# Kernel optimization log

Measured on AMD Instinct MI355X. Metric: run time of the kernel, lower is better.

The kernel has to match this reference:

```python
import jax, jax.numpy as jnp
import numpy as np

N = 100000   # nodes
E = 1600000  # edges (avg degree 16)
D = 128      # in_dim == hidden_dim (required by residual + shared BN)
G = 64       # graphs in the batch
EPS = 1e-5   # BatchNorm eps


def setup_inputs() -> dict:
    key = jax.random.key(0)
    ks = jax.random.split(key, 10)
    h = jax.random.normal(ks[0], (N, D), jnp.float32)
    src = jax.random.randint(ks[1], (E,), 0, N)
    dst = jax.random.randint(ks[2], (E,), 0, N)
    graph_ids = jnp.sort(jax.random.randint(ks[3], (N,), 0, G))
    s = 1.0 / np.sqrt(D)
    W1 = jax.random.uniform(ks[4], (D, D), jnp.float32, -s, s)
    b1 = jnp.zeros((D,), jnp.float32)
    W2 = jax.random.uniform(ks[5], (D, D), jnp.float32, -s, s)
    b2 = jnp.zeros((D,), jnp.float32)
    gate_W = jax.random.uniform(ks[6], (D, 1), jnp.float32, -s, s)
    gate_b = jnp.zeros((1,), jnp.float32)
    gamma = jnp.ones((D,), jnp.float32)
    beta = jnp.zeros((D,), jnp.float32)
    return {"h": h, "src": src, "dst": dst, "graph_ids": graph_ids,
            "num_graphs": G, "W1": W1, "b1": b1, "W2": W2, "b2": b2,
            "gate_W": gate_W, "gate_b": gate_b, "gamma": gamma, "beta": beta}


def reference(h, src, dst, graph_ids, num_graphs, W1, b1, W2, b2, gate_W, gate_b, gamma, beta):
    n = h.shape[0]

    # dgl.mean_nodes: per-graph mean of initial features
    node_counts = jnp.clip(jax.ops.segment_sum(jnp.ones((n,), h.dtype), graph_ids, num_graphs), 1.0)
    init_avg_h = jax.ops.segment_sum(h, graph_ids, num_graphs) / node_counts[:, None]

    # training-mode BatchNorm1d with shared gamma/beta (same bn module used twice)
    def bn(x):
        m = jnp.mean(x, axis=0)
        v = jnp.mean(jnp.square(x - m), axis=0)  # biased variance (torch BN)
        return (x - m) * jax.lax.rsqrt(v + EPS) * gamma + beta

    ones_e = jnp.ones(src.shape[0], h.dtype)
    deg_out = jnp.clip(jax.ops.segment_sum(ones_e, src, n), 1.0)  # out-degree of src
    deg_in = jnp.clip(jax.ops.segment_sum(ones_e, dst, n), 1.0)   # in-degree of dst
    inv_sqrt_out = jax.lax.rsqrt(deg_out)[:, None]
    inv_sqrt_in = jax.lax.rsqrt(deg_in)[:, None]

    # DGL GraphConv, norm='both': D_dst^{-1/2} A (D_src^{-1/2} x) W + b
    def graph_conv(x, W, b):
        xs = x * inv_sqrt_out
        agg = jax.ops.segment_sum(xs[src], dst, n)  # SpMM: gather src, scatter-add at dst
        return (agg * inv_sqrt_in) @ W + b

    h1 = h + jax.nn.relu(graph_conv(bn(h), W1, b1))
    h2 = h1 + jax.nn.relu(graph_conv(bn(h1), W2, b2))

    # GlobalAttentionPooling: per-graph softmax over gate scores, weighted sum of h2
    gate = h2 @ gate_W + gate_b  # [N, 1]
    gmax = jax.ops.segment_max(gate, graph_ids, num_graphs)
    e = jnp.exp(gate - gmax[graph_ids])
    denom = jax.ops.segment_sum(e, graph_ids, num_graphs)
    alpha = e / denom[graph_ids]
    hg = jax.ops.segment_sum(alpha * h2, graph_ids, num_graphs)  # [G, D]

    return hg, init_avg_h
```

## Files before the change

kernel.cpp:

```cpp
#include <hip/hip_runtime.h>
#include <math.h>

#define N_NODES 100000
#define N_EDGES 1600000
#define DIM     128
#define NG      64
#define BN_EPS  1e-5f
#define NB      98
#define HRANGE  12500
#define NSLICE  32
#define ESLICE  (N_EDGES / NSLICE)
#define NBLK_CONV 1563
#define SB      128
#define NSB     782

typedef __attribute__((ext_vector_type(8))) short bf16x8;
typedef __attribute__((ext_vector_type(4))) float f32x4;

__device__ __forceinline__ unsigned short f2bf(float f) {
  unsigned b = __float_as_uint(f);
  unsigned r = (b + 0x7FFFu + ((b >> 16) & 1u)) >> 16;
  return (unsigned short)r;
}

__launch_bounds__(1024)
__global__ void k_histO(const int* __restrict__ src, int* __restrict__ cntO) {
  __shared__ int histo[HRANGE];
  int t = threadIdx.x;
  int range = blockIdx.x >> 5, blk = blockIdx.x & 31;
  int lo = range * HRANGE;
  for (int j = t; j < HRANGE; j += 1024) histo[j] = 0;
  __syncthreads();
  const int4* sp = (const int4*)(src + blk * ESLICE);
  for (int q = t; q < ESLICE / 4; q += 1024) {
    int4 v = sp[q];
    unsigned a = (unsigned)(v.x - lo), b = (unsigned)(v.y - lo);
    unsigned c = (unsigned)(v.z - lo), d = (unsigned)(v.w - lo);
    if (a < (unsigned)HRANGE) atomicAdd(&histo[a], 1);
    if (b < (unsigned)HRANGE) atomicAdd(&histo[b], 1);
    if (c < (unsigned)HRANGE) atomicAdd(&histo[c], 1);
    if (d < (unsigned)HRANGE) atomicAdd(&histo[d], 1);
  }
  __syncthreads();
  for (int j = t; j < HRANGE; j += 1024) {
    int v = histo[j];
    if (v) atomicAdd(&cntO[lo + j], v);
  }
}

__launch_bounds__(1024)
__global__ void k_histD(const int* __restrict__ dst, int* __restrict__ cnt_slice) {
  __shared__ int histo[HRANGE];
  int t = threadIdx.x;
  int range = blockIdx.x >> 5, slice = blockIdx.x & 31;
  int lo = range * HRANGE;
  for (int j = t; j < HRANGE; j += 1024) histo[j] = 0;
  __syncthreads();
  const int4* dp = (const int4*)(dst + slice * ESLICE);
  for (int q = t; q < ESLICE / 4; q += 1024) {
    int4 v = dp[q];
    unsigned a = (unsigned)(v.x - lo), b = (unsigned)(v.y - lo);
    unsigned c = (unsigned)(v.z - lo), d = (unsigned)(v.w - lo);
    if (a < (unsigned)HRANGE) atomicAdd(&histo[a], 1);
    if (b < (unsigned)HRANGE) atomicAdd(&histo[b], 1);
    if (c < (unsigned)HRANGE) atomicAdd(&histo[c], 1);
    if (d < (unsigned)HRANGE) atomicAdd(&histo[d], 1);
  }
  __syncthreads();
  for (int j = t; j < HRANGE; j += 1024)
    cnt_slice[(size_t)slice * N_NODES + lo + j] = histo[j];
}

__global__ void k_scan_part(int* __restrict__ cnt_slice, int* __restrict__ cnt,
                            int* __restrict__ bsum) {
  int b = blockIdx.x, t = threadIdx.x;
  int base = b * 1024 + t * 4;
  int tot = 0;
#pragma unroll
  for (int j = 0; j < 4; ++j) {
    int i = base + j;
    if (i < N_NODES) {
      int run = 0;
#pragma unroll
      for (int s = 0; s < NSLICE; ++s) {
        int v = cnt_slice[(size_t)s * N_NODES + i];
        cnt_slice[(size_t)s * N_NODES + i] = run;
        run += v;
      }
      cnt[i] = run;
      tot += run;
    }
  }
  __shared__ int red[256];
  red[t] = tot; __syncthreads();
  for (int w = 128; w; w >>= 1) { if (t < w) red[t] += red[t + w]; __syncthreads(); }
  if (t == 0) bsum[b] = red[0];
}

__global__ void k_scan_mid(const int* __restrict__ bsum, int* __restrict__ boff,
                           int* __restrict__ rowstart) {
  int t = threadIdx.x;
  __shared__ int sh[128];
  int own = (t < NB) ? bsum[t] : 0;
  sh[t] = own;
  __syncthreads();
  for (int off = 1; off < 128; off <<= 1) {
    int v = (t >= off) ? sh[t - off] : 0;
    __syncthreads();
    sh[t] += v;
    __syncthreads();
  }
  if (t < NB) boff[t] = sh[t] - own;
  if (t == NB - 1) rowstart[N_NODES] = sh[t];
}

__global__ void k_scan_fin(const int* __restrict__ cnt, const int* __restrict__ boff,
                           int* __restrict__ rowstart) {
  int b = blockIdx.x, t = threadIdx.x;
  int base = b * 1024 + t * 4;
  int v0 = 0, v1 = 0, v2 = 0, v3 = 0;
  if (base + 0 < N_NODES) v0 = cnt[base + 0];
  if (base + 1 < N_NODES) v1 = cnt[base + 1];
  if (base + 2 < N_NODES) v2 = cnt[base + 2];
  if (base + 3 < N_NODES) v3 = cnt[base + 3];
  int tsum = v0 + v1 + v2 + v3;
  __shared__ int sh[256];
  sh[t] = tsum;
  __syncthreads();
  for (int off = 1; off < 256; off <<= 1) {
    int v = (t >= off) ? sh[t - off] : 0;
    __syncthreads();
    sh[t] += v;
    __syncthreads();
  }
  int run = boff[b] + sh[t] - tsum;
  if (base + 0 < N_NODES) rowstart[base + 0] = run; run += v0;
  if (base + 1 < N_NODES) rowstart[base + 1] = run; run += v1;
  if (base + 2 < N_NODES) rowstart[base + 2] = run; run += v2;
  if (base + 3 < N_NODES) rowstart[base + 3] = run;
}

__launch_bounds__(1024)
__global__ void k_scatter_slice(const int* __restrict__ src, const int* __restrict__ dst,
                                const int* __restrict__ rowstart,
                                const int* __restrict__ cnt_slice, int* __restrict__ csr) {
  __shared__ int cur[HRANGE];
  int t = threadIdx.x;
  int range = blockIdx.x >> 5, slice = blockIdx.x & 31;
  int lo = range * HRANGE;
  for (int j = t; j < HRANGE; j += 1024)
    cur[j] = rowstart[lo + j] + cnt_slice[(size_t)slice * N_NODES + lo + j];
  __syncthreads();
  const int4* dp = (const int4*)(dst + slice * ESLICE);
  const int4* sp = (const int4*)(src + slice * ESLICE);
  for (int q = t; q < ESLICE / 4; q += 1024) {
    int4 d = dp[q];
    int4 s = sp[q];
    unsigned o;
    o = (unsigned)(d.x - lo); if (o < (unsigned)HRANGE) { int p = atomicAdd(&cur[o], 1); csr[p] = s.x; }
    o = (unsigned)(d.y - lo); if (o < (unsigned)HRANGE) { int p = atomicAdd(&cur[o], 1); csr[p] = s.y; }
    o = (unsigned)(d.z - lo); if (o < (unsigned)HRANGE) { int p = atomicAdd(&cur[o], 1); csr[p] = s.z; }
    o = (unsigned)(d.w - lo); if (o < (unsigned)HRANGE) { int p = atomicAdd(&cur[o], 1); csr[p] = s.w; }
  }
}

__global__ void k_starts_fill(const int* __restrict__ gid, int* __restrict__ starts) {
  int i = blockIdx.x * blockDim.x + threadIdx.x;
  if (i >= N_NODES) return;
  int gi = gid[i];
  if (i == 0) {
    for (int g = 0; g <= gi; ++g) starts[g] = 0;
  } else {
    int gp = gid[i - 1];
    if (gp != gi) for (int g = gp + 1; g <= gi; ++g) starts[g] = i;
  }
  if (i == N_NODES - 1) {
    for (int g = gi + 1; g <= NG; ++g) starts[g] = N_NODES;
  }
}

__launch_bounds__(256)
__global__ void k_stats1(const float* __restrict__ x, const int* __restrict__ gid,
                         float* __restrict__ sums, float* __restrict__ initavg) {
  __shared__ float ls[8][DIM];
  __shared__ float ls2[8][DIM];
  __shared__ float lseg[4][8][DIM];
  int t = threadIdx.x;
  int col4 = (t & 31) * 4, rg = t >> 5;
  for (int i = t; i < 4 * 8 * DIM; i += 256) ((float*)lseg)[i] = 0.f;
  int base = blockIdx.x * SB;
  int rend = min(base + SB, N_NODES);
  int g0 = gid[base];
  int gl = gid[rend - 1];
  __syncthreads();
  float4 s = {0.f,0.f,0.f,0.f}, s2 = {0.f,0.f,0.f,0.f};
  float4 acc = {0.f,0.f,0.f,0.f};
  if (g0 == gl) {
    for (int r = base + rg; r < rend; r += 8) {
      float4 v = *(const float4*)&x[(size_t)r * DIM + col4];
      s.x += v.x; s.y += v.y; s.z += v.z; s.w += v.w;
      s2.x += v.x*v.x; s2.y += v.y*v.y; s2.z += v.z*v.z; s2.w += v.w*v.w;
      acc.x += v.x; acc.y += v.y; acc.z += v.z; acc.w += v.w;
    }
    lseg[0][rg][col4+0] = acc.x; lseg[0][rg][col4+1] = acc.y;
    lseg[0][rg][col4+2] = acc.z; lseg[0][rg][col4+3] = acc.w;
  } else {
    int curg = g0;
    for (int r = base + rg; r < rend; r += 8) {
      float4 v = *(const float4*)&x[(size_t)r * DIM + col4];
      s.x += v.x; s.y += v.y; s.z += v.z; s.w += v.w;
      s2.x += v.x*v.x; s2.y += v.y*v.y; s2.z += v.z*v.z; s2.w += v.w*v.w;
      int g = gid[r];
      if (g != curg) {
        int slot = curg - g0;
        if (slot < 4) {
          lseg[slot][rg][col4+0] = acc.x; lseg[slot][rg][col4+1] = acc.y;
          lseg[slot][rg][col4+2] = acc.z; lseg[slot][rg][col4+3] = acc.w;
        } else {
          atomicAdd(&initavg[curg * DIM + col4+0], acc.x);
          atomicAdd(&initavg[curg * DIM + col4+1], acc.y);
          atomicAdd(&initavg[curg * DIM + col4+2], acc.z);
          atomicAdd(&initavg[curg * DIM + col4+3], acc.w);
        }
        acc.x = acc.y = acc.z = acc.w = 0.f;
        curg = g;
      }
      acc.x += v.x; acc.y += v.y; acc.z += v.z; acc.w += v.w;
    }
    int slot = curg - g0;
    if (slot < 4) {
      lseg[slot][rg][col4+0] = acc.x; lseg[slot][rg][col4+1] = acc.y;
      lseg[slot][rg][col4+2] = acc.z; lseg[slot][rg][col4+3] = acc.w;
    } else {
      atomicAdd(&initavg[curg * DIM + col4+0], acc.x);
      atomicAdd(&initavg[curg * DIM + col4+1], acc.y);
      atomicAdd(&initavg[curg * DIM + col4+2], acc.z);
      atomicAdd(&initavg[curg * DIM + col4+3], acc.w);
    }
  }
  *(float4*)&ls[rg][col4] = s;
  *(float4*)&ls2[rg][col4] = s2;
  __syncthreads();
  if (t < DIM) {
    float a = 0.f, b = 0.f;
#pragma unroll
    for (int j = 0; j < 8; ++j) { a += ls[j][t]; b += ls2[j][t]; }
    atomicAdd(&sums[t], a);
    atomicAdd(&sums[DIM + t], b);
#pragma unroll
    for (int slot = 0; slot < 4; ++slot) {
      float v = 0.f;
#pragma unroll
      for (int j = 0; j < 8; ++j) v += lseg[slot][j][t];
      int g = g0 + slot;
      if (g < NG && v != 0.f) atomicAdd(&initavg[g * DIM + t], v);
    }
  }
}

__global__ void k_avg_div(const int* __restrict__ starts, float* __restrict__ outp) {
  int g = blockIdx.x, d = threadIdx.x;
  float cnt = fmaxf((float)(starts[g + 1] - starts[g]), 1.0f);
  outp[g * DIM + d] /= cnt;
}

__global__ void k_colred(const float* __restrict__ psum, const float* __restrict__ psq,
                         float* __restrict__ sums) {
  int c = blockIdx.x, t = threadIdx.x;
  __shared__ float r1[256], r2[256];
  float a = 0.f, b = 0.f;
  for (int j = t; j < NBLK_CONV; j += 256) {
    a += psum[(size_t)c * NBLK_CONV + j];
    b += psq[(size_t)c * NBLK_CONV + j];
  }
  r1[t] = a; r2[t] = b; __syncthreads();
  for (int w = 128; w; w >>= 1) { if (t < w) { r1[t] += r1[t + w]; r2[t] += r2[t + w]; } __syncthreads(); }
  if (t == 0) { sums[c] = r1[0]; sums[DIM + c] = r2[0]; }
}

__launch_bounds__(256)
__global__ void k_bnx(const float* __restrict__ x, const float* __restrict__ sums,
                      const float* __restrict__ gamma, const float* __restrict__ beta,
                      const int* __restrict__ cntO, unsigned short* __restrict__ xb) {
  int idx = blockIdx.x * 256 + threadIdx.x;
  int row = idx >> 5, c4 = (idx & 31) * 4;
  float4 sm = *(const float4*)&sums[c4];
  float4 sq = *(const float4*)&sums[DIM + c4];
  float4 ga = *(const float4*)&gamma[c4];
  float4 be = *(const float4*)&beta[c4];
  const float inv = 1.0f / N_NODES;
  float4 sc, sh;
  {
    float m = sm.x * inv, va = sq.x * inv - m * m;
    sc.x = rsqrtf(fmaxf(va, 0.f) + BN_EPS) * ga.x; sh.x = be.x - m * sc.x;
    m = sm.y * inv; va = sq.y * inv - m * m;
    sc.y = rsqrtf(fmaxf(va, 0.f) + BN_EPS) * ga.y; sh.y = be.y - m * sc.y;
    m = sm.z * inv; va = sq.z * inv - m * m;
    sc.z = rsqrtf(fmaxf(va, 0.f) + BN_EPS) * ga.z; sh.z = be.z - m * sc.z;
    m = sm.w * inv; va = sq.w * inv - m * m;
    sc.w = rsqrtf(fmaxf(va, 0.f) + BN_EPS) * ga.w; sh.w = be.w - m * sc.w;
  }
  float4 v = *(const float4*)&x[(size_t)row * DIM + c4];
  float f = rsqrtf(fmaxf((float)cntO[row], 1.0f));
  ushort4 o;
  o.x = f2bf((v.x * sc.x + sh.x) * f);
  o.y = f2bf((v.y * sc.y + sh.y) * f);
  o.z = f2bf((v.z * sc.z + sh.z) * f);
  o.w = f2bf((v.w * sc.w + sh.w) * f);
  *(ushort4*)&xb[(size_t)row * DIM + c4] = o;
}

__global__ void k_prepW(const float* __restrict__ W1, const float* __restrict__ W2,
                        unsigned short* __restrict__ WbT1, unsigned short* __restrict__ WbT2) {
  int idx = blockIdx.x * 256 + threadIdx.x;
  int which = idx >> 14;
  int i = idx & 16383;
  int k = i >> 7, c = i & 127;
  const float* W = which ? W2 : W1;
  unsigned short* O = which ? WbT2 : WbT1;
  O[c * DIM + k] = f2bf(W[k * DIM + c]);
}

__launch_bounds__(256, 8)
__global__ void k_spmm_pull(const unsigned short* __restrict__ xb, const int* __restrict__ csr,
                            const int* __restrict__ rowstart, unsigned short* __restrict__ aggb) {
  int row = blockIdx.x * 4 + threadIdx.y;
  int l = threadIdx.x;
  int half = l >> 5, l32 = l & 31;
  int s = rowstart[row], e = rowstart[row + 1];
  float4 acc = {0.f, 0.f, 0.f, 0.f};
  const size_t coff = (size_t)l32 * 4;
  int i = s + half;
  for (; i + 14 < e; i += 16) {
    int s0 = csr[i],      s1 = csr[i + 2],  s2 = csr[i + 4],  s3 = csr[i + 6];
    int s4 = csr[i + 8],  s5 = csr[i + 10], s6 = csr[i + 12], s7 = csr[i + 14];
    uint2 w0 = *(const uint2*)&xb[(size_t)s0 * DIM + coff];
    uint2 w1 = *(const uint2*)&xb[(size_t)s1 * DIM + coff];
    uint2 w2 = *(const uint2*)&xb[(size_t)s2 * DIM + coff];
    uint2 w3 = *(const uint2*)&xb[(size_t)s3 * DIM + coff];
    uint2 w4 = *(const uint2*)&xb[(size_t)s4 * DIM + coff];
    uint2 w5 = *(const uint2*)&xb[(size_t)s5 * DIM + coff];
    uint2 w6 = *(const uint2*)&xb[(size_t)s6 * DIM + coff];
    uint2 w7 = *(const uint2*)&xb[(size_t)s7 * DIM + coff];
    acc.x += (__uint_as_float(w0.x << 16) + __uint_as_float(w1.x << 16))
           + (__uint_as_float(w2.x << 16) + __uint_as_float(w3.x << 16))
           + (__uint_as_float(w4.x << 16) + __uint_as_float(w5.x << 16))
           + (__uint_as_float(w6.x << 16) + __uint_as_float(w7.x << 16));
    acc.y += (__uint_as_float(w0.x & 0xFFFF0000u) + __uint_as_float(w1.x & 0xFFFF0000u))
           + (__uint_as_float(w2.x & 0xFFFF0000u) + __uint_as_float(w3.x & 0xFFFF0000u))
           + (__uint_as_float(w4.x & 0xFFFF0000u) + __uint_as_float(w5.x & 0xFFFF0000u))
           + (__uint_as_float(w6.x & 0xFFFF0000u) + __uint_as_float(w7.x & 0xFFFF0000u));
    acc.z += (__uint_as_float(w0.y << 16) + __uint_as_float(w1.y << 16))
           + (__uint_as_float(w2.y << 16) + __uint_as_float(w3.y << 16))
           + (__uint_as_float(w4.y << 16) + __uint_as_float(w5.y << 16))
           + (__uint_as_float(w6.y << 16) + __uint_as_float(w7.y << 16));
    acc.w += (__uint_as_float(w0.y & 0xFFFF0000u) + __uint_as_float(w1.y & 0xFFFF0000u))
           + (__uint_as_float(w2.y & 0xFFFF0000u) + __uint_as_float(w3.y & 0xFFFF0000u))
           + (__uint_as_float(w4.y & 0xFFFF0000u) + __uint_as_float(w5.y & 0xFFFF0000u))
           + (__uint_as_float(w6.y & 0xFFFF0000u) + __uint_as_float(w7.y & 0xFFFF0000u));
  }
  for (; i + 6 < e; i += 8) {
    int s0 = csr[i], s1 = csr[i + 2], s2 = csr[i + 4], s3 = csr[i + 6];
    uint2 w0 = *(const uint2*)&xb[(size_t)s0 * DIM + coff];
    uint2 w1 = *(const uint2*)&xb[(size_t)s1 * DIM + coff];
    uint2 w2 = *(const uint2*)&xb[(size_t)s2 * DIM + coff];
    uint2 w3 = *(const uint2*)&xb[(size_t)s3 * DIM + coff];
    acc.x += __uint_as_float(w0.x << 16) + __uint_as_float(w1.x << 16)
           + __uint_as_float(w2.x << 16) + __uint_as_float(w3.x << 16);
    acc.y += __uint_as_float(w0.x & 0xFFFF0000u) + __uint_as_float(w1.x & 0xFFFF0000u)
           + __uint_as_float(w2.x & 0xFFFF0000u) + __uint_as_float(w3.x & 0xFFFF0000u);
    acc.z += __uint_as_float(w0.y << 16) + __uint_as_float(w1.y << 16)
           + __uint_as_float(w2.y << 16) + __uint_as_float(w3.y << 16);
    acc.w += __uint_as_float(w0.y & 0xFFFF0000u) + __uint_as_float(w1.y & 0xFFFF0000u)
           + __uint_as_float(w2.y & 0xFFFF0000u) + __uint_as_float(w3.y & 0xFFFF0000u);
  }
  for (; i < e; i += 2) {
    int s0 = csr[i];
    uint2 w0 = *(const uint2*)&xb[(size_t)s0 * DIM + coff];
    acc.x += __uint_as_float(w0.x << 16);
    acc.y += __uint_as_float(w0.x & 0xFFFF0000u);
    acc.z += __uint_as_float(w0.y << 16);
    acc.w += __uint_as_float(w0.y & 0xFFFF0000u);
  }
  acc.x += __shfl_xor(acc.x, 32);
  acc.y += __shfl_xor(acc.y, 32);
  acc.z += __shfl_xor(acc.z, 32);
  acc.w += __shfl_xor(acc.w, 32);
  if (half == 0) {
    float isi = rsqrtf(fmaxf((float)(e - s), 1.0f));
    ushort4 o;
    o.x = f2bf(acc.x * isi);
    o.y = f2bf(acc.y * isi);
    o.z = f2bf(acc.z * isi);
    o.w = f2bf(acc.w * isi);
    *(ushort4*)&aggb[(size_t)row * DIM + l32 * 4] = o;
  }
}

__launch_bounds__(256)
__global__ void k_conv(const unsigned short* __restrict__ aggb,
                       const unsigned short* __restrict__ WbT,
                       const float* __restrict__ bias, const float* __restrict__ hres,
                       float* __restrict__ outp,
                       const float* __restrict__ gWp, const float* __restrict__ gbp,
                       float* __restrict__ gatep,
                       float* __restrict__ psum, float* __restrict__ psq) {
  __shared__ unsigned short As[64 * 136];
  __shared__ unsigned short Ws[128 * 136];
  __shared__ float gsh[64];
  float* Of = (float*)Ws;
  int t = threadIdx.x;
  int row0 = blockIdx.x * 64;

  if (gatep && t < 64) gsh[t] = 0.f;

  for (int i = t; i < 1024; i += 256) {
    int r = i >> 4, q = i & 15;
    int row = row0 + r;
    int4 v = {0, 0, 0, 0};
    if (row < N_NODES) v = *(const int4*)&aggb[(size_t)row * DIM + q * 8];
    *(int4*)&As[r * 136 + q * 8] = v;
  }
  for (int i = t; i < 2048; i += 256) {
    int c = i >> 4, q = i & 15;
    *(int4*)&Ws[c * 136 + q * 8] = *(const int4*)&WbT[(size_t)c * DIM + q * 8];
  }
  __syncthreads();

  int wid = t >> 6, l = t & 63;
  int wr = wid >> 1, wc = wid & 1;
  int lr = l & 15, lq = l >> 4;
  f32x4 acc[2][4] = {};
  const unsigned short* Ab = &As[(wr * 32 + lr) * 136 + lq * 8];
  const unsigned short* Bb = &Ws[(wc * 64 + lr) * 136 + lq * 8];
#pragma unroll
  for (int kk = 0; kk < 4; ++kk) {
    bf16x8 a0 = *(const bf16x8*)(Ab + kk * 32);
    bf16x8 a1 = *(const bf16x8*)(Ab + 16 * 136 + kk * 32);
    bf16x8 b0 = *(const bf16x8*)(Bb + kk * 32);
    bf16x8 b1 = *(const bf16x8*)(Bb + 16 * 136 + kk * 32);
    bf16x8 b2 = *(const bf16x8*)(Bb + 32 * 136 + kk * 32);
    bf16x8 b3 = *(const bf16x8*)(Bb + 48 * 136 + kk * 32);
    acc[0][0] = __builtin_amdgcn_mfma_f32_16x16x32_bf16(a0, b0, acc[0][0], 0, 0, 0);
    acc[0][1] = __builtin_amdgcn_mfma_f32_16x16x32_bf16(a0, b1, acc[0][1], 0, 0, 0);
    acc[0][2] = __builtin_amdgcn_mfma_f32_16x16x32_bf16(a0, b2, acc[0][2], 0, 0, 0);
    acc[0][3] = __builtin_amdgcn_mfma_f32_16x16x32_bf16(a0, b3, acc[0][3], 0, 0, 0);
    acc[1][0] = __builtin_amdgcn_mfma_f32_16x16x32_bf16(a1, b0, acc[1][0], 0, 0, 0);
    acc[1][1] = __builtin_amdgcn_mfma_f32_16x16x32_bf16(a1, b1, acc[1][1], 0, 0, 0);
    acc[1][2] = __builtin_amdgcn_mfma_f32_16x16x32_bf16(a1, b2, acc[1][2], 0, 0, 0);
    acc[1][3] = __builtin_amdgcn_mfma_f32_16x16x32_bf16(a1, b3, acc[1][3], 0, 0, 0);
  }
  __syncthreads();

#pragma unroll
  for (int rt = 0; rt < 2; ++rt) {
#pragma unroll
    for (int ct = 0; ct < 4; ++ct) {
      int rr = wr * 32 + rt * 16 + lq * 4;
      int cc = wc * 64 + ct * 16 + lr;
#pragma unroll
      for (int i = 0; i < 4; ++i)
        Of[(rr + i) * 132 + cc] = acc[rt][ct][i];
    }
  }
  __syncthreads();

  float st[4] = {0.f, 0.f, 0.f, 0.f}, st2[4] = {0.f, 0.f, 0.f, 0.f};
#pragma unroll
  for (int i = 0; i < 8; ++i) {
    int fi = t + i * 256;
    int r = fi >> 5, c4 = (fi & 31) * 4;
    int row = row0 + r;
    if (row < N_NODES) {
      float4 o  = *(float4*)&Of[r * 132 + c4];
      float4 bv = *(const float4*)&bias[c4];
      float4 hv = *(const float4*)&hres[(size_t)row * DIM + c4];
      float4 y = {hv.x + fmaxf(o.x + bv.x, 0.f), hv.y + fmaxf(o.y + bv.y, 0.f),
                  hv.z + fmaxf(o.z + bv.z, 0.f), hv.w + fmaxf(o.w + bv.w, 0.f)};
      *(float4*)&outp[(size_t)row * DIM + c4] = y;
      if (gatep) {
        float4 gw = *(const float4*)&gWp[c4];
        atomicAdd(&gsh[r], y.x * gw.x + y.y * gw.y + y.z * gw.z + y.w * gw.w);
      }
      if (psum) {
        st[0] += y.x; st[1] += y.y; st[2] += y.z; st[3] += y.w;
        st2[0] += y.x*y.x; st2[1] += y.y*y.y; st2[2] += y.z*y.z; st2[3] += y.w*y.w;
      }
    }
  }
  if (gatep) {
    __syncthreads();
    int row = row0 + t;
    if (t < 64 && row < N_NODES) gatep[row] = gsh[t] + gbp[0];
  }
  if (psum) {
    float* sls  = (float*)As;
    float* sls2 = sls + 8 * DIM;
    int rg = t >> 5, c4 = (t & 31) * 4;
    __syncthreads();
#pragma unroll
    for (int i = 0; i < 4; ++i) {
      sls[rg * DIM + c4 + i]  = st[i];
      sls2[rg * DIM + c4 + i] = st2[i];
    }
    __syncthreads();
    if (t < DIM) {
      float a = 0.f, b = 0.f;
#pragma unroll
      for (int j = 0; j < 8; ++j) { a += sls[j * DIM + t]; b += sls2[j * DIM + t]; }
      psum[(size_t)t * NBLK_CONV + blockIdx.x] = a;
      psq[(size_t)t * NBLK_CONV + blockIdx.x]  = b;
    }
  }
}

__global__ void k_gstats(const float* __restrict__ gate, const int* __restrict__ starts,
                         float* __restrict__ gmax, float* __restrict__ gden) {
  int g = blockIdx.x;
  int s = starts[g], e = starts[g + 1];
  int t = threadIdx.x;
  __shared__ float red[256];
  float m = -INFINITY;
  for (int i = s + t; i < e; i += 256) m = fmaxf(m, gate[i]);
  red[t] = m; __syncthreads();
  for (int w = 128; w; w >>= 1) { if (t < w) red[t] = fmaxf(red[t], red[t + w]); __syncthreads(); }
  float mg = red[0]; __syncthreads();
  float ssum = 0.f;
  for (int i = s + t; i < e; i += 256) ssum += expf(gate[i] - mg);
  red[t] = ssum; __syncthreads();
  for (int w = 128; w; w >>= 1) { if (t < w) red[t] += red[t + w]; __syncthreads(); }
  if (t == 0) { gmax[g] = mg; gden[g] = red[0]; }
}

__launch_bounds__(256)
__global__ void k_pool(const float* __restrict__ h2, const float* __restrict__ gate,
                       const int* __restrict__ starts, const float* __restrict__ gmax,
                       const float* __restrict__ gden, float* __restrict__ outp) {
  __shared__ float ls[8][DIM];
  int g = blockIdx.x >> 5, part = blockIdx.x & 31;
  int s = starts[g], e = starts[g + 1];
  int t = threadIdx.x;
  int col4 = (t & 31) * 4, rg = t >> 5;
  float mg = gmax[g];
  float dn = gden[g];
  float invden = dn > 0.f ? 1.0f / dn : 0.f;
  float4 acc = {0.f, 0.f, 0.f, 0.f};
  for (int i = s + part + rg * 32; i < e; i += 256) {
    float w = expf(gate[i] - mg) * invden;
    float4 v = *(const float4*)&h2[(size_t)i * DIM + col4];
    acc.x += w * v.x; acc.y += w * v.y; acc.z += w * v.z; acc.w += w * v.w;
  }
  *(float4*)&ls[rg][col4] = acc;
  __syncthreads();
  if (t < DIM) {
    float a = 0.f;
#pragma unroll
    for (int j = 0; j < 8; ++j) a += ls[j][t];
    if (a != 0.f) atomicAdd(&outp[g * DIM + t], a);
  }
}

extern "C" void kernel_launch(void* const* d_in, const int* in_sizes, int n_in,
                              void* d_out, int out_size, void* d_ws, size_t ws_size,
                              hipStream_t stream) {
  const float* h    = (const float*)d_in[0];
  const int*   src  = (const int*)d_in[1];
  const int*   dst  = (const int*)d_in[2];
  const int*   gid  = (const int*)d_in[3];
  const float* W1   = (const float*)d_in[5];
  const float* b1   = (const float*)d_in[6];
  const float* W2   = (const float*)d_in[7];
  const float* b2   = (const float*)d_in[8];
  const float* gW   = (const float*)d_in[9];
  const float* gb   = (const float*)d_in[10];
  const float* gamma= (const float*)d_in[11];
  const float* beta = (const float*)d_in[12];
  float* out = (float*)d_out;

  char* ws = (char*)d_ws;
  float* h12     = (float*)ws; ws += (size_t)N_NODES * DIM * 4;
  unsigned short* xb   = (unsigned short*)ws; ws += (size_t)N_NODES * DIM * 2;
  unsigned short* aggb = (unsigned short*)ws; ws += (size_t)N_NODES * DIM * 2;
  int*   csr     = (int*)ws;   ws += (size_t)N_EDGES * 4;
  int*   cnt_slice = (int*)ws; ws += (size_t)NSLICE * N_NODES * 4;
  float* psum    = (float*)ws; ws += (size_t)DIM * NBLK_CONV * 4;
  float* psq     = (float*)ws; ws += (size_t)DIM * NBLK_CONV * 4;
  unsigned short* WbT1 = (unsigned short*)ws; ws += DIM * DIM * 2;
  unsigned short* WbT2 = (unsigned short*)ws; ws += DIM * DIM * 2;
  int*   rowstart= (int*)ws;   ws += (N_NODES + 1) * 4;
  int*   cnt     = (int*)ws;   ws += N_NODES * 4;
  int*   cntO    = (int*)ws;   ws += N_NODES * 4;
  float* gate    = (float*)ws; ws += N_NODES * 4;
  float* sums    = (float*)ws; ws += 2 * DIM * 4;
  float* gmax    = (float*)ws; ws += NG * 4;
  float* gden    = (float*)ws; ws += NG * 4;
  int*   starts  = (int*)ws;   ws += (NG + 1) * 4;
  int*   bsum    = (int*)ws;   ws += NB * 4;
  int*   boff    = (int*)ws;   ws += NB * 4;

  hipMemsetAsync(cntO,  0, N_NODES * 4, stream);
  hipMemsetAsync(sums,  0, 2 * DIM * 4, stream);
  hipMemsetAsync(d_out, 0, (size_t)out_size * 4, stream);

  k_histO<<<256, 1024, 0, stream>>>(src, cntO);
  k_histD<<<256, 1024, 0, stream>>>(dst, cnt_slice);
  k_scan_part<<<NB, 256, 0, stream>>>(cnt_slice, cnt, bsum);
  k_scan_mid<<<1, 128, 0, stream>>>(bsum, boff, rowstart);
  k_scan_fin<<<NB, 256, 0, stream>>>(cnt, boff, rowstart);
  k_scatter_slice<<<256, 1024, 0, stream>>>(src, dst, rowstart, cnt_slice, csr);
  k_starts_fill<<<(N_NODES + 255) / 256, 256, 0, stream>>>(gid, starts);
  k_prepW<<<128, 256, 0, stream>>>(W1, W2, WbT1, WbT2);

  k_stats1<<<NSB, 256, 0, stream>>>(h, gid, sums, out + NG * DIM);
  k_avg_div<<<NG, DIM, 0, stream>>>(starts, out + NG * DIM);
  k_bnx<<<N_NODES * 32 / 256, 256, 0, stream>>>(h, sums, gamma, beta, cntO, xb);
  k_spmm_pull<<<N_NODES / 4, dim3(64, 4), 0, stream>>>(xb, csr, rowstart, aggb);
  k_conv<<<NBLK_CONV, 256, 0, stream>>>(aggb, WbT1, b1, h, h12,
                                        nullptr, nullptr, nullptr, psum, psq);

  k_colred<<<DIM, 256, 0, stream>>>(psum, psq, sums);
  k_bnx<<<N_NODES * 32 / 256, 256, 0, stream>>>(h12, sums, gamma, beta, cntO, xb);
  k_spmm_pull<<<N_NODES / 4, dim3(64, 4), 0, stream>>>(xb, csr, rowstart, aggb);
  k_conv<<<NBLK_CONV, 256, 0, stream>>>(aggb, WbT2, b2, h12, h12,
                                        gW, gb, gate, nullptr, nullptr);

  k_gstats<<<NG, 256, 0, stream>>>(gate, starts, gmax, gden);
  k_pool<<<NG * 32, 256, 0, stream>>>(h12, gate, starts, gmax, gden, out);
}
```

Baseline: 369.6 us.

## Fuse SpMM aggregation into the conv GEMM kernel via shared memory

Merges the pull-style sparse aggregation into the MFMA conv kernel. Each 64-row block now gathers neighbour features for its own rows and writes the bf16 aggregate straight into shared memory, so the intermediate aggb buffer never goes to global memory and one launch per layer disappears. In exchange, each wave processes 16 rows one after another with only 4-way unrolled gathers instead of the 8-way variant. The kernel also carries large LDS usage, which may limit how much memory-latency hiding the gather phase gets.

```diff
diff --git a/kernel.cpp b/kernel.cpp
--- a/kernel.cpp
+++ b/kernel.cpp
@@ -321,90 +321,15 @@
   O[c * DIM + k] = f2bf(W[k * DIM + c]);
 }
 
-__launch_bounds__(256, 8)
-__global__ void k_spmm_pull(const unsigned short* __restrict__ xb, const int* __restrict__ csr,
-                            const int* __restrict__ rowstart, unsigned short* __restrict__ aggb) {
-  int row = blockIdx.x * 4 + threadIdx.y;
-  int l = threadIdx.x;
-  int half = l >> 5, l32 = l & 31;
-  int s = rowstart[row], e = rowstart[row + 1];
-  float4 acc = {0.f, 0.f, 0.f, 0.f};
-  const size_t coff = (size_t)l32 * 4;
-  int i = s + half;
-  for (; i + 14 < e; i += 16) {
-    int s0 = csr[i],      s1 = csr[i + 2],  s2 = csr[i + 4],  s3 = csr[i + 6];
-    int s4 = csr[i + 8],  s5 = csr[i + 10], s6 = csr[i + 12], s7 = csr[i + 14];
-    uint2 w0 = *(const uint2*)&xb[(size_t)s0 * DIM + coff];
-    uint2 w1 = *(const uint2*)&xb[(size_t)s1 * DIM + coff];
-    uint2 w2 = *(const uint2*)&xb[(size_t)s2 * DIM + coff];
-    uint2 w3 = *(const uint2*)&xb[(size_t)s3 * DIM + coff];
-    uint2 w4 = *(const uint2*)&xb[(size_t)s4 * DIM + coff];
-    uint2 w5 = *(const uint2*)&xb[(size_t)s5 * DIM + coff];
-    uint2 w6 = *(const uint2*)&xb[(size_t)s6 * DIM + coff];
-    uint2 w7 = *(const uint2*)&xb[(size_t)s7 * DIM + coff];
-    acc.x += (__uint_as_float(w0.x << 16) + __uint_as_float(w1.x << 16))
-           + (__uint_as_float(w2.x << 16) + __uint_as_float(w3.x << 16))
-           + (__uint_as_float(w4.x << 16) + __uint_as_float(w5.x << 16))
-           + (__uint_as_float(w6.x << 16) + __uint_as_float(w7.x << 16));
-    acc.y += (__uint_as_float(w0.x & 0xFFFF0000u) + __uint_as_float(w1.x & 0xFFFF0000u))
-           + (__uint_as_float(w2.x & 0xFFFF0000u) + __uint_as_float(w3.x & 0xFFFF0000u))
-           + (__uint_as_float(w4.x & 0xFFFF0000u) + __uint_as_float(w5.x & 0xFFFF0000u))
-           + (__uint_as_float(w6.x & 0xFFFF0000u) + __uint_as_float(w7.x & 0xFFFF0000u));
-    acc.z += (__uint_as_float(w0.y << 16) + __uint_as_float(w1.y << 16))
-           + (__uint_as_float(w2.y << 16) + __uint_as_float(w3.y << 16))
-           + (__uint_as_float(w4.y << 16) + __uint_as_float(w5.y << 16))
-           + (__uint_as_float(w6.y << 16) + __uint_as_float(w7.y << 16));
-    acc.w += (__uint_as_float(w0.y & 0xFFFF0000u) + __uint_as_float(w1.y & 0xFFFF0000u))
-           + (__uint_as_float(w2.y & 0xFFFF0000u) + __uint_as_float(w3.y & 0xFFFF0000u))
-           + (__uint_as_float(w4.y & 0xFFFF0000u) + __uint_as_float(w5.y & 0xFFFF0000u))
-           + (__uint_as_float(w6.y & 0xFFFF0000u) + __uint_as_float(w7.y & 0xFFFF0000u));
-  }
-  for (; i + 6 < e; i += 8) {
-    int s0 = csr[i], s1 = csr[i + 2], s2 = csr[i + 4], s3 = csr[i + 6];
-    uint2 w0 = *(const uint2*)&xb[(size_t)s0 * DIM + coff];
-    uint2 w1 = *(const uint2*)&xb[(size_t)s1 * DIM + coff];
-    uint2 w2 = *(const uint2*)&xb[(size_t)s2 * DIM + coff];
-    uint2 w3 = *(const uint2*)&xb[(size_t)s3 * DIM + coff];
-    acc.x += __uint_as_float(w0.x << 16) + __uint_as_float(w1.x << 16)
-           + __uint_as_float(w2.x << 16) + __uint_as_float(w3.x << 16);
-    acc.y += __uint_as_float(w0.x & 0xFFFF0000u) + __uint_as_float(w1.x & 0xFFFF0000u)
-           + __uint_as_float(w2.x & 0xFFFF0000u) + __uint_as_float(w3.x & 0xFFFF0000u);
-    acc.z += __uint_as_float(w0.y << 16) + __uint_as_float(w1.y << 16)
-           + __uint_as_float(w2.y << 16) + __uint_as_float(w3.y << 16);
-    acc.w += __uint_as_float(w0.y & 0xFFFF0000u) + __uint_as_float(w1.y & 0xFFFF0000u)
-           + __uint_as_float(w2.y & 0xFFFF0000u) + __uint_as_float(w3.y & 0xFFFF0000u);
-  }
-  for (; i < e; i += 2) {
-    int s0 = csr[i];
-    uint2 w0 = *(const uint2*)&xb[(size_t)s0 * DIM + coff];
-    acc.x += __uint_as_float(w0.x << 16);
-    acc.y += __uint_as_float(w0.x & 0xFFFF0000u);
-    acc.z += __uint_as_float(w0.y << 16);
-    acc.w += __uint_as_float(w0.y & 0xFFFF0000u);
-  }
-  acc.x += __shfl_xor(acc.x, 32);
-  acc.y += __shfl_xor(acc.y, 32);
-  acc.z += __shfl_xor(acc.z, 32);
-  acc.w += __shfl_xor(acc.w, 32);
-  if (half == 0) {
-    float isi = rsqrtf(fmaxf((float)(e - s), 1.0f));
-    ushort4 o;
-    o.x = f2bf(acc.x * isi);
-    o.y = f2bf(acc.y * isi);
-    o.z = f2bf(acc.z * isi);
-    o.w = f2bf(acc.w * isi);
-    *(ushort4*)&aggb[(size_t)row * DIM + l32 * 4] = o;
-  }
-}
-
 __launch_bounds__(256)
-__global__ void k_conv(const unsigned short* __restrict__ aggb,
-                       const unsigned short* __restrict__ WbT,
-                       const float* __restrict__ bias, const float* __restrict__ hres,
-                       float* __restrict__ outp,
-                       const float* __restrict__ gWp, const float* __restrict__ gbp,
-                       float* __restrict__ gatep,
-                       float* __restrict__ psum, float* __restrict__ psq) {
+__global__ void k_spmmconv(const unsigned short* __restrict__ xb, const int* __restrict__ csr,
+                           const int* __restrict__ rowstart,
+                           const unsigned short* __restrict__ WbT,
+                           const float* __restrict__ bias, const float* __restrict__ hres,
+                           float* __restrict__ outp,
+                           const float* __restrict__ gWp, const float* __restrict__ gbp,
+                           float* __restrict__ gatep,
+                           float* __restrict__ psum, float* __restrict__ psq) {
   __shared__ unsigned short As[64 * 136];
   __shared__ unsigned short Ws[128 * 136];
   __shared__ float gsh[64];
@@ -414,20 +339,60 @@
 
   if (gatep && t < 64) gsh[t] = 0.f;
 
-  for (int i = t; i < 1024; i += 256) {
-    int r = i >> 4, q = i & 15;
-    int row = row0 + r;
-    int4 v = {0, 0, 0, 0};
-    if (row < N_NODES) v = *(const int4*)&aggb[(size_t)row * DIM + q * 8];
-    *(int4*)&As[r * 136 + q * 8] = v;
-  }
   for (int i = t; i < 2048; i += 256) {
     int c = i >> 4, q = i & 15;
     *(int4*)&Ws[c * 136 + q * 8] = *(const int4*)&WbT[(size_t)c * DIM + q * 8];
   }
-  __syncthreads();
 
   int wid = t >> 6, l = t & 63;
+  int half = l >> 5, l32 = l & 31;
+  const size_t coff = (size_t)l32 * 4;
+  for (int r = 0; r < 16; ++r) {
+    int rl = wid * 16 + r;
+    int row = row0 + rl;
+    int s = 0, e = 0;
+    if (row < N_NODES) { s = rowstart[row]; e = rowstart[row + 1]; }
+    float4 acc = {0.f, 0.f, 0.f, 0.f};
+    int i = s + half;
+    for (; i + 6 < e; i += 8) {
+      int s0 = csr[i], s1 = csr[i + 2], s2 = csr[i + 4], s3 = csr[i + 6];
+      uint2 w0 = *(const uint2*)&xb[(size_t)s0 * DIM + coff];
+      uint2 w1 = *(const uint2*)&xb[(size_t)s1 * DIM + coff];
+      uint2 w2 = *(const uint2*)&xb[(size_t)s2 * DIM + coff];
+      uint2 w3 = *(const uint2*)&xb[(size_t)s3 * DIM + coff];
+      acc.x += __uint_as_float(w0.x << 16) + __uint_as_float(w1.x << 16)
+             + __uint_as_float(w2.x << 16) + __uint_as_float(w3.x << 16);
+      acc.y += __uint_as_float(w0.x & 0xFFFF0000u) + __uint_as_float(w1.x & 0xFFFF0000u)
+             + __uint_as_float(w2.x & 0xFFFF0000u) + __uint_as_float(w3.x & 0xFFFF0000u);
+      acc.z += __uint_as_float(w0.y << 16) + __uint_as_float(w1.y << 16)
+             + __uint_as_float(w2.y << 16) + __uint_as_float(w3.y << 16);
+      acc.w += __uint_as_float(w0.y & 0xFFFF0000u) + __uint_as_float(w1.y & 0xFFFF0000u)
+             + __uint_as_float(w2.y & 0xFFFF0000u) + __uint_as_float(w3.y & 0xFFFF0000u);
+    }
+    for (; i < e; i += 2) {
+      int s0 = csr[i];
+      uint2 w0 = *(const uint2*)&xb[(size_t)s0 * DIM + coff];
+      acc.x += __uint_as_float(w0.x << 16);
+      acc.y += __uint_as_float(w0.x & 0xFFFF0000u);
+      acc.z += __uint_as_float(w0.y << 16);
+      acc.w += __uint_as_float(w0.y & 0xFFFF0000u);
+    }
+    acc.x += __shfl_xor(acc.x, 32);
+    acc.y += __shfl_xor(acc.y, 32);
+    acc.z += __shfl_xor(acc.z, 32);
+    acc.w += __shfl_xor(acc.w, 32);
+    if (half == 0) {
+      float isi = rsqrtf(fmaxf((float)(e - s), 1.0f));
+      ushort4 o;
+      o.x = f2bf(acc.x * isi);
+      o.y = f2bf(acc.y * isi);
+      o.z = f2bf(acc.z * isi);
+      o.w = f2bf(acc.w * isi);
+      *(ushort4*)&As[rl * 136 + l32 * 4] = o;
+    }
+  }
+  __syncthreads();
+
   int wr = wid >> 1, wc = wid & 1;
   int lr = l & 15, lq = l >> 4;
   f32x4 acc[2][4] = {};
@@ -580,7 +545,6 @@
   char* ws = (char*)d_ws;
   float* h12     = (float*)ws; ws += (size_t)N_NODES * DIM * 4;
   unsigned short* xb   = (unsigned short*)ws; ws += (size_t)N_NODES * DIM * 2;
-  unsigned short* aggb = (unsigned short*)ws; ws += (size_t)N_NODES * DIM * 2;
   int*   csr     = (int*)ws;   ws += (size_t)N_EDGES * 4;
   int*   cnt_slice = (int*)ws; ws += (size_t)NSLICE * N_NODES * 4;
   float* psum    = (float*)ws; ws += (size_t)DIM * NBLK_CONV * 4;
@@ -614,15 +578,13 @@
   k_stats1<<<NSB, 256, 0, stream>>>(h, gid, sums, out + NG * DIM);
   k_avg_div<<<NG, DIM, 0, stream>>>(starts, out + NG * DIM);
   k_bnx<<<N_NODES * 32 / 256, 256, 0, stream>>>(h, sums, gamma, beta, cntO, xb);
-  k_spmm_pull<<<N_NODES / 4, dim3(64, 4), 0, stream>>>(xb, csr, rowstart, aggb);
-  k_conv<<<NBLK_CONV, 256, 0, stream>>>(aggb, WbT1, b1, h, h12,
-                                        nullptr, nullptr, nullptr, psum, psq);
+  k_spmmconv<<<NBLK_CONV, 256, 0, stream>>>(xb, csr, rowstart, WbT1, b1, h, h12,
+                                            nullptr, nullptr, nullptr, psum, psq);
 
   k_colred<<<DIM, 256, 0, stream>>>(psum, psq, sums);
   k_bnx<<<N_NODES * 32 / 256, 256, 0, stream>>>(h12, sums, gamma, beta, cntO, xb);
-  k_spmm_pull<<<N_NODES / 4, dim3(64, 4), 0, stream>>>(xb, csr, rowstart, aggb);
-  k_conv<<<NBLK_CONV, 256, 0, stream>>>(aggb, WbT2, b2, h12, h12,
-                                        gW, gb, gate, nullptr, nullptr);
+  k_spmmconv<<<NBLK_CONV, 256, 0, stream>>>(xb, csr, rowstart, WbT2, b2, h12, h12,
+                                            gW, gb, gate, nullptr, nullptr);
 
   k_gstats<<<NG, 256, 0, stream>>>(gate, starts, gmax, gden);
   k_pool<<<NG * 32, 256, 0, stream>>>(h12, gate, starts, gmax, gden, out);
```

New measurement: 498.7 us. +34.9%, slower.
